# Performance work log

Measured on AMD Instinct MI355X. Metric: run time of the kernel, lower is better.

The kernel has to match this reference:

```python
import jax, jax.numpy as jnp
import numpy as np

BATCH, SEQ, IN, HID, OUT = 64, 512, 512, 1024, 512


def setup_inputs() -> dict:
    key = jax.random.key(0)
    ks = jax.random.split(key, 7)
    s_ih = 1.0 / np.sqrt(IN)
    s_hh = 1.0 / np.sqrt(HID)
    return {
        "x_sequence": jax.random.normal(ks[0], (BATCH, SEQ, IN), dtype=jnp.float32),
        "W_ih": jax.random.uniform(ks[1], (HID, IN), jnp.float32, -s_ih, s_ih),
        "b_ih": jax.random.uniform(ks[2], (HID,), jnp.float32, -s_ih, s_ih),
        "W_hh": jax.random.uniform(ks[3], (HID, HID), jnp.float32, -s_hh, s_hh),
        "b_hh": jax.random.uniform(ks[4], (HID,), jnp.float32, -s_hh, s_hh),
        "W_ho": jax.random.uniform(ks[5], (OUT, HID), jnp.float32, -s_hh, s_hh),
        "b_ho": jax.random.uniform(ks[6], (OUT,), jnp.float32, -s_hh, s_hh),
    }


def reference(x_sequence, W_ih, b_ih, W_hh, b_hh, W_ho, b_ho):
    # Elman RNN: h_t = tanh(x_t @ W_ih^T + b_ih + h_{t-1} @ W_hh^T + b_hh)
    # Returned output is the projection of the FINAL hidden state only
    # (per-step outputs in the original are detached bookkeeping).
    # Precompute all input projections in one big GEMM: [B,S,H]
    x_proj = jnp.einsum("bsi,hi->bsh", x_sequence, W_ih) + b_ih + b_hh

    def step(h, xp_t):
        h_new = jnp.tanh(xp_t + h @ W_hh.T)
        return h_new, None

    h0 = jnp.zeros((x_sequence.shape[0], W_hh.shape[0]), dtype=x_sequence.dtype)
    h_final, _ = jax.lax.scan(step, h0, jnp.swapaxes(x_proj, 0, 1))  # scan over time
    output = h_final @ W_ho.T + b_ho  # [B, OUT]
    return output
```

## Files before the change

kernel.cpp:

```cpp
#include <hip/hip_runtime.h>
#include <cstdint>
#include <cstddef>

typedef unsigned short ushort_t;
typedef unsigned int uint_t;
typedef unsigned long long u64_t;
typedef __attribute__((ext_vector_type(8))) short frag16;
typedef __attribute__((ext_vector_type(8))) unsigned short u16x8;
typedef __attribute__((ext_vector_type(4))) float f32x4;

#define SEQ   512
#define INF   512
#define HID   1024
#define OUTF  512
#define NB     4
#define RPB    64
#define WSTR   1040
#define SPIN_LIMIT (1 << 18)

__device__ __forceinline__ float b2f(ushort_t u) {
    union { unsigned int i; float f; } v; v.i = ((unsigned int)u) << 16; return v.f;
}
__device__ __forceinline__ ushort_t f2b(float f) {
    unsigned int u = __float_as_uint(f);
    unsigned int r = (u + 0x7fffu + ((u >> 16) & 1u)) >> 16;
    return (ushort_t)r;
}
__device__ __forceinline__ float fast_tanh(float s) {
    const float e = __expf(2.0f * s);
    return 1.0f - 2.0f * __builtin_amdgcn_rcpf(e + 1.0f);
}

__device__ __forceinline__ void lds_barrier() {
    asm volatile("s_waitcnt lgkmcnt(0)" ::: "memory");
    __builtin_amdgcn_sched_barrier(0);
    __builtin_amdgcn_s_barrier();
    __builtin_amdgcn_sched_barrier(0);
}

__device__ __forceinline__ void cvt8_hilo(const float* __restrict__ src, u16x8* hi, u16x8* lo) {
    const float4 x0 = *(const float4*)src;
    const float4 x1 = *(const float4*)(src + 4);
    float xs[8] = {x0.x,x0.y,x0.z,x0.w,x1.x,x1.y,x1.z,x1.w};
    u16x8 h, l;
#pragma unroll
    for (int j = 0; j < 8; ++j) {
        const ushort_t hb = f2b(xs[j]);
        h[j] = hb;
        l[j] = f2b(xs[j] - b2f(hb));
    }
    *hi = h; if (lo) *lo = l;
}
__device__ __forceinline__ u16x8 cvt8_hi(const float* __restrict__ src) {
    const float4 x0 = *(const float4*)src;
    const float4 x1 = *(const float4*)(src + 4);
    float xs[8] = {x0.x,x0.y,x0.z,x0.w,x1.x,x1.y,x1.z,x1.w};
    u16x8 h;
#pragma unroll
    for (int j = 0; j < 8; ++j) h[j] = f2b(xs[j]);
    return h;
}

__global__ __launch_bounds__(256, 2)
void xproj_kernel(const float* __restrict__ X, const float* __restrict__ Wih,
                  const float* __restrict__ bih, const float* __restrict__ bhh,
                  float* __restrict__ XP)
{
    __shared__ ushort_t Ah[128][40];
    __shared__ ushort_t Al[128][40];
    __shared__ ushort_t Bs[128][40];
    const int tid = (int)threadIdx.x;
    const int m0 = (int)blockIdx.x * 128;
    const int n0 = (int)blockIdx.y * 128;
    const int w  = tid >> 6, l = tid & 63;
    const int wm = (w & 1) * 64, wn = (w >> 1) * 64;
    const int lm = l & 15, lg = l >> 4, hk = lg * 8;
    const int sr = tid >> 2, sc = (tid & 3) * 8;

    f32x4 acc[4][4];
#pragma unroll
    for (int a = 0; a < 4; ++a)
#pragma unroll
        for (int b = 0; b < 4; ++b) { acc[a][b][0]=0.f; acc[a][b][1]=0.f; acc[a][b][2]=0.f; acc[a][b][3]=0.f; }

    for (int ko = 0; ko < INF; ko += 32) {
        __syncthreads();
        u16x8 h, lo;
        cvt8_hilo(&X[(size_t)(m0+sr)*INF + ko + sc], &h, &lo);
        *(u16x8*)&Ah[sr][sc] = h;  *(u16x8*)&Al[sr][sc] = lo;
        cvt8_hilo(&X[(size_t)(m0+sr+64)*INF + ko + sc], &h, &lo);
        *(u16x8*)&Ah[sr+64][sc] = h;  *(u16x8*)&Al[sr+64][sc] = lo;
        *(u16x8*)&Bs[sr][sc]    = cvt8_hi(&Wih[(size_t)(n0+sr)*INF + ko + sc]);
        *(u16x8*)&Bs[sr+64][sc] = cvt8_hi(&Wih[(size_t)(n0+sr+64)*INF + ko + sc]);
        __syncthreads();
        frag16 afh[4], afl[4], bf[4];
#pragma unroll
        for (int i = 0; i < 4; ++i) afh[i] = *(const frag16*)&Ah[wm + i*16 + lm][hk];
#pragma unroll
        for (int i = 0; i < 4; ++i) afl[i] = *(const frag16*)&Al[wm + i*16 + lm][hk];
#pragma unroll
        for (int i = 0; i < 4; ++i) bf[i]  = *(const frag16*)&Bs[wn + i*16 + lm][hk];
#pragma unroll
        for (int a = 0; a < 4; ++a)
#pragma unroll
            for (int b = 0; b < 4; ++b) {
                acc[a][b] = __builtin_amdgcn_mfma_f32_16x16x32_bf16(afh[a], bf[b], acc[a][b], 0, 0, 0);
                acc[a][b] = __builtin_amdgcn_mfma_f32_16x16x32_bf16(afl[a], bf[b], acc[a][b], 0, 0, 0);
            }
    }

#pragma unroll
    for (int b = 0; b < 4; ++b) {
        const int n = n0 + wn + b*16 + lm;
        const float bias = bih[n] + bhh[n];
#pragma unroll
        for (int a = 0; a < 4; ++a)
#pragma unroll
            for (int q = 0; q < 4; ++q) {
                const int m = m0 + wm + a*16 + lg*4 + q;
                XP[(size_t)m * HID + n] = acc[a][b][q] + bias;
            }
    }
}

__global__ __launch_bounds__(256, 1)
void rnn_scan_kernel(const float* __restrict__ XP, const float* __restrict__ Whh,
                     u64_t* __restrict__ Hbuf)
{
    __shared__ ushort_t Ws[RPB][WSTR];
    __shared__ ushort_t Hhi[NB][WSTR];
    __shared__ ushort_t Hlo[NB][WSTR];
    __shared__ float    Cred[2][4][4][4][16];

    const int tid = (int)threadIdx.x;
    const int w = tid >> 6, l = tid & 63;
    const int lm = l & 15, lg = l >> 4;
    const int bid = (int)blockIdx.x;
    const int gid = (bid & 7) * 2 + ((bid >> 3) & 1);
    const int r   = bid >> 4;
    const int b0 = gid * NB;
    const int j0 = r * RPB;
    const int qcol = w * 256;
    const int jcol = j0 + w*16 + lm;
    const int bq   = b0 + lg;

    {
        const int rr = tid >> 2, cq = (tid & 3) * 256;
        const float* src = Whh + (size_t)(j0 + rr) * HID + cq;
#pragma unroll
        for (int i = 0; i < 32; ++i)
            *(u16x8*)&Ws[rr][cq + i*8] = cvt8_hi(&src[i*8]);
    }
    lds_barrier();

    int goff[16];
#pragma unroll
    for (int j = 0; j < 16; ++j)
        goff[j] = (b0 + (j & 3)) * 1024 + qcol + ((j >> 2) << 6) + l;

    u64_t v[16];
    float xpv, xpn;

    {
        xpv = XP[(size_t)((bq) * SEQ + 0) * HID + jcol];
        const float hv = fast_tanh(xpv);
        const ushort_t hi = f2b(hv);
        const ushort_t lo = f2b(hv - b2f(hi));
        const u64_t pk = ((u64_t)((uint_t)hi | ((uint_t)lo << 16)) << 32) | 1ull;
#pragma unroll
        for (int j = 0; j < 16; ++j)
            v[j] = __hip_atomic_load(&Hbuf[goff[j]], __ATOMIC_RELAXED,
                                     __HIP_MEMORY_SCOPE_AGENT);
        xpn = XP[(size_t)((bq) * SEQ + 1) * HID + jcol];
        __hip_atomic_store(&Hbuf[(size_t)bq * 1024 + jcol], pk,
                           __ATOMIC_RELAXED, __HIP_MEMORY_SCOPE_AGENT);
    }

    for (int t = 1; t < SEQ; ++t) {
        xpv = xpn;
        {
            const u64_t* base = Hbuf + (size_t)((t - 1) & 1) * 65536;
            const uint_t want = (uint_t)t;
            int spin = 0;
            for (;;) {
                int bad = 0;
#pragma unroll
                for (int j = 0; j < 16; ++j) bad |= ((uint_t)v[j] != want);
                if (!__any(bad)) break;
                if (++spin > SPIN_LIMIT) break;
#pragma unroll
                for (int j = 0; j < 16; ++j)
                    if ((uint_t)v[j] != want)
                        v[j] = __hip_atomic_load(&base[goff[j]], __ATOMIC_RELAXED,
                                                 __HIP_MEMORY_SCOPE_AGENT);
            }
        }

#pragma unroll
        for (int j = 0; j < 16; ++j) {
            const uint_t d = (uint_t)(v[j] >> 32);
            const int c = qcol + ((j >> 2) << 6) + l;
            Hhi[j & 3][c] = (ushort_t)(d & 0xffffu);
            Hlo[j & 3][c] = (ushort_t)(d >> 16);
        }
        asm volatile("s_waitcnt lgkmcnt(0)" ::: "memory");
        __builtin_amdgcn_sched_barrier(0);

        f32x4 acc[4];
#pragma unroll
        for (int i = 0; i < 4; ++i) { acc[i][0]=0.f; acc[i][1]=0.f; acc[i][2]=0.f; acc[i][3]=0.f; }
        {
            const int kbase = qcol + lg * 8;
            const ushort_t* ph = &Hhi[lm & 3][kbase];
            const ushort_t* pl = &Hlo[lm & 3][kbase];
            const ushort_t* pw = &Ws[lm][kbase];
#pragma unroll
            for (int kk = 0; kk < 256; kk += 32) {
                const frag16 ahi = *(const frag16*)(ph + kk);
                const frag16 alo = *(const frag16*)(pl + kk);
#pragma unroll
                for (int tl = 0; tl < 4; ++tl) {
                    const frag16 wf = *(const frag16*)(pw + (size_t)tl * 16 * WSTR + kk);
                    acc[tl] = __builtin_amdgcn_mfma_f32_16x16x32_bf16(ahi, wf, acc[tl], 0, 0, 0);
                    acc[tl] = __builtin_amdgcn_mfma_f32_16x16x32_bf16(alo, wf, acc[tl], 0, 0, 0);
                }
            }
        }
#pragma unroll
        for (int q = 0; q < 4; ++q)
            Cred[t & 1][w][lg][q][lm] = acc[lg][q];
        lds_barrier();

        const float s = (Cred[t & 1][0][w][lg][lm] + Cred[t & 1][1][w][lg][lm])
                      + (Cred[t & 1][2][w][lg][lm] + Cred[t & 1][3][w][lg][lm]);
        const float hv = fast_tanh(s + xpv);
        const ushort_t hi = f2b(hv);
        const ushort_t lo = f2b(hv - b2f(hi));
        const u64_t pk = ((u64_t)((uint_t)hi | ((uint_t)lo << 16)) << 32)
                       | (u64_t)(uint_t)(t + 1);

        if (t + 1 < SEQ) {
            const u64_t* base = Hbuf + (size_t)(t & 1) * 65536;
#pragma unroll
            for (int j = 0; j < 16; ++j)
                v[j] = __hip_atomic_load(&base[goff[j]], __ATOMIC_RELAXED,
                                         __HIP_MEMORY_SCOPE_AGENT);
            xpn = XP[(size_t)((bq) * SEQ + (t + 1)) * HID + jcol];
        }
        __hip_atomic_store(&Hbuf[((size_t)(t & 1) * 64 + bq) * 1024 + jcol], pk,
                           __ATOMIC_RELAXED, __HIP_MEMORY_SCOPE_AGENT);
    }
}

__global__ __launch_bounds__(256)
void outproj_kernel(const u64_t* __restrict__ Hp, const float* __restrict__ Who,
                    const float* __restrict__ bho, float* __restrict__ Out)
{
    const int tid = (int)threadIdx.x;
    const int w = tid >> 6, l = tid & 63;
    const int lm = l & 15, lg = l >> 4, hk = lg * 8;
    const int n0 = (int)blockIdx.x * 64;

    f32x4 acc[4];
#pragma unroll
    for (int i = 0; i < 4; ++i) { acc[i][0]=0.f; acc[i][1]=0.f; acc[i][2]=0.f; acc[i][3]=0.f; }

    for (int k0 = 0; k0 < HID; k0 += 32) {
        const u64_t* hr = Hp + (size_t)(w*16 + lm) * HID + k0 + hk;
        frag16 ahi, alo;
#pragma unroll
        for (int j = 0; j < 8; ++j) {
            const uint_t d = (uint_t)(hr[j] >> 32);
            ahi[j] = (short)(d & 0xffffu);
            alo[j] = (short)(d >> 16);
        }
#pragma unroll
        for (int bi = 0; bi < 4; ++bi) {
            const u16x8 bv = cvt8_hi(&Who[(size_t)(n0 + bi*16 + lm) * HID + k0 + hk]);
            acc[bi] = __builtin_amdgcn_mfma_f32_16x16x32_bf16(ahi, (frag16)bv, acc[bi], 0, 0, 0);
            acc[bi] = __builtin_amdgcn_mfma_f32_16x16x32_bf16(alo, (frag16)bv, acc[bi], 0, 0, 0);
        }
    }
#pragma unroll
    for (int bi = 0; bi < 4; ++bi) {
        const int n = n0 + bi*16 + lm;
        const float bias = bho[n];
#pragma unroll
        for (int q = 0; q < 4; ++q) {
            const int b = w*16 + lg*4 + q;
            Out[(size_t)b * OUTF + n] = acc[bi][q] + bias;
        }
    }
}

extern "C" void kernel_launch(void* const* d_in, const int* in_sizes, int n_in,
                              void* d_out, int out_size, void* d_ws, size_t ws_size,
                              hipStream_t stream)
{
    const float* X   = (const float*)d_in[0];
    const float* Wih = (const float*)d_in[1];
    const float* bih = (const float*)d_in[2];
    const float* Whh = (const float*)d_in[3];
    const float* bhh = (const float*)d_in[4];
    const float* Who = (const float*)d_in[5];
    const float* bho = (const float*)d_in[6];
    float* Out = (float*)d_out;

    char* ws = (char*)d_ws;
    float* XP = (float*)ws;
    u64_t* Hbuf = (u64_t*)(ws + (size_t)32768 * 1024 * 4);

    xproj_kernel<<<dim3(256, 8), dim3(256), 0, stream>>>(X, Wih, bih, bhh, XP);

    rnn_scan_kernel<<<dim3(256), dim3(256), 0, stream>>>(XP, Whh, Hbuf);

    outproj_kernel<<<dim3(OUTF / 64), dim3(256), 0, stream>>>(Hbuf + (size_t)64 * 1024,
                                                              Who, bho, Out);
}
```

Measured before the change: 2.053 ms.

## Add heater wavefront burning FMAs while the scan spins on cross-block sync

Adds a fifth wavefront per scan block that runs dummy FMA chains while the compute waves wait for the previous step's hidden state, stopping once all four waves report arrival through an LDS counter. The intent is to keep the compute units busy so clocks stay high during the latency-bound per-step synchronisation. This adds power draw and extra barrier participation, and the barrier counts must match between the heater wave and the compute waves or the block can hang or misbehave.

```diff
diff --git a/kernel.cpp b/kernel.cpp
--- a/kernel.cpp
+++ b/kernel.cpp
@@ -17,6 +17,7 @@
 #define RPB    64
 #define WSTR   1040
 #define SPIN_LIMIT (1 << 18)
+#define HEAT_CHUNK_LIMIT (1 << 14)
 
 __device__ __forceinline__ float b2f(ushort_t u) {
     union { unsigned int i; float f; } v; v.i = ((unsigned int)u) << 16; return v.f;
@@ -37,6 +38,17 @@
     __builtin_amdgcn_s_barrier();
     __builtin_amdgcn_sched_barrier(0);
 }
+
+#define BURN16(z0,z1,z2,z3) \
+    asm volatile("v_fmac_f32 %0, %4, %0\n\tv_fmac_f32 %1, %4, %1\n\t"  \
+                 "v_fmac_f32 %2, %4, %2\n\tv_fmac_f32 %3, %4, %3\n\t"  \
+                 "v_fmac_f32 %0, %4, %0\n\tv_fmac_f32 %1, %4, %1\n\t"  \
+                 "v_fmac_f32 %2, %4, %2\n\tv_fmac_f32 %3, %4, %3\n\t"  \
+                 "v_fmac_f32 %0, %4, %0\n\tv_fmac_f32 %1, %4, %1\n\t"  \
+                 "v_fmac_f32 %2, %4, %2\n\tv_fmac_f32 %3, %4, %3\n\t"  \
+                 "v_fmac_f32 %0, %4, %0\n\tv_fmac_f32 %1, %4, %1\n\t"  \
+                 "v_fmac_f32 %2, %4, %2\n\tv_fmac_f32 %3, %4, %3"      \
+                 : "+v"(z0), "+v"(z1), "+v"(z2), "+v"(z3) : "v"(1e-30f))
 
 __device__ __forceinline__ void cvt8_hilo(const float* __restrict__ src, u16x8* hi, u16x8* lo) {
     const float4 x0 = *(const float4*)src;
@@ -123,7 +135,7 @@
     }
 }
 
-__global__ __launch_bounds__(256, 1)
+__global__ __launch_bounds__(320, 1)
 void rnn_scan_kernel(const float* __restrict__ XP, const float* __restrict__ Whh,
                      u64_t* __restrict__ Hbuf)
 {
@@ -131,9 +143,33 @@
     __shared__ ushort_t Hhi[NB][WSTR];
     __shared__ ushort_t Hlo[NB][WSTR];
     __shared__ float    Cred[2][4][4][4][16];
+    __shared__ int      Sdone;
 
     const int tid = (int)threadIdx.x;
     const int w = tid >> 6, l = tid & 63;
+
+    if (tid == 0) Sdone = 0;
+
+    if (w == 4) {
+        float z0 = 1.0f + (float)(l & 3), z1 = 2.0f, z2 = 3.0f, z3 = 4.0f;
+        lds_barrier();
+        for (int t = 1; t < SEQ; ++t) {
+            const int goal = 4 * t;
+            int it = 0;
+            while (it < HEAT_CHUNK_LIMIT) {
+                if (__hip_atomic_load(&Sdone, __ATOMIC_RELAXED,
+                                      __HIP_MEMORY_SCOPE_WORKGROUP) >= goal)
+                    break;
+                BURN16(z0,z1,z2,z3); BURN16(z0,z1,z2,z3);
+                BURN16(z0,z1,z2,z3); BURN16(z0,z1,z2,z3);
+                ++it;
+            }
+            lds_barrier();
+        }
+        asm volatile("" :: "v"(z0), "v"(z1), "v"(z2), "v"(z3));
+        return;
+    }
+
     const int lm = l & 15, lg = l >> 4;
     const int bid = (int)blockIdx.x;
     const int gid = (bid & 7) * 2 + ((bid >> 3) & 1);
@@ -195,6 +231,9 @@
                                                  __HIP_MEMORY_SCOPE_AGENT);
             }
         }
+        if (l == 0)
+            __hip_atomic_fetch_add(&Sdone, 1, __ATOMIC_RELAXED,
+                                   __HIP_MEMORY_SCOPE_WORKGROUP);
 
 #pragma unroll
         for (int j = 0; j < 16; ++j) {
@@ -312,7 +351,7 @@
 
     xproj_kernel<<<dim3(256, 8), dim3(256), 0, stream>>>(X, Wih, bih, bhh, XP);
 
-    rnn_scan_kernel<<<dim3(256), dim3(256), 0, stream>>>(XP, Whh, Hbuf);
+    rnn_scan_kernel<<<dim3(256), dim3(320), 0, stream>>>(XP, Whh, Hbuf);
 
     outproj_kernel<<<dim3(OUTF / 64), dim3(256), 0, stream>>>(Hbuf + (size_t)64 * 1024,
                                                               Who, bho, Out);
```

After: 2.085 ms. About the same (+1.5%).
